# Kernel optimization log

Measured on AMD Instinct MI355X. Metric: run time of the kernel, lower is better.

The kernel has to match this reference:

```python
import jax, jax.numpy as jnp
import numpy as np
import math

BSZ, H, P, L = 8, 512, 256, 4096
DT_MIN, DT_MAX = 1e-3, 1e-1


def setup_inputs() -> dict:
    key = jax.random.key(0)
    ks = jax.random.split(key, 7)
    input_sequence = jax.random.normal(ks[0], (BSZ, 1, H, 1, L), dtype=jnp.float32)
    # HiPPO-like init: negative real parts, spread imaginary parts
    Lambda_re = -(0.1 + jax.random.uniform(ks[1], (P,), dtype=jnp.float32))  # in (-1.1, -0.1)
    Lambda_im = jax.random.normal(ks[2], (P,), dtype=jnp.float32) * math.pi
    B = jax.random.normal(ks[3], (P, H, 2), dtype=jnp.float32) / math.sqrt(H)
    C = jax.random.normal(ks[4], (H, P, 2), dtype=jnp.float32) * (0.5 ** 0.5)
    D = jax.random.normal(ks[5], (H,), dtype=jnp.float32)
    u = jax.random.uniform(ks[6], (P, 1), dtype=jnp.float32)
    log_step = math.log(DT_MIN) + u * (math.log(DT_MAX) - math.log(DT_MIN))
    return {"input_sequence": input_sequence, "Lambda_re": Lambda_re,
            "Lambda_im": Lambda_im, "B": B, "C": C, "D": D, "log_step": log_step}


def _binary_operator(q_i, q_j):
    A_i, b_i = q_i
    A_j, b_j = q_j
    return (A_j * A_i, A_j * b_i + b_j)


def reference(input_sequence, Lambda_re, Lambda_im, B, C, D, log_step):
    # conj_sym=True, clip_eigs=False, activation='gelu'
    Lambda = Lambda_re + 1j * Lambda_im                       # (P,) complex
    B_tilde = B[..., 0] + 1j * B[..., 1]                      # (P,H)
    C_tilde = C[..., 0] + 1j * C[..., 1]                      # (H,P)
    step = jnp.exp(log_step[:, 0])                            # (P,)
    # ZOH discretization
    Lambda_bar = jnp.exp(Lambda * step)                       # (P,)
    B_bar = ((Lambda_bar - 1.0) / Lambda)[:, None] * B_tilde  # (P,H)
    # (bsz,1,H,1,L) -> (bsz,L,H)
    u = input_sequence[:, 0, :, 0].transpose(0, 2, 1)
    Bu = jnp.einsum('ph,blh->blp', B_bar, u.astype(B_bar.dtype))  # (bsz,L,P) complex
    Lambda_elems = jnp.broadcast_to(Lambda_bar, Bu.shape)
    _, xs = jax.lax.associative_scan(_binary_operator, (Lambda_elems, Bu), axis=1)
    ys = 2.0 * jnp.einsum('hp,blp->blh', C_tilde, xs).real    # conj_sym output
    ys = ys + u * D                                           # feedthrough
    ys = jax.nn.gelu(ys, approximate=False)
    return ys.transpose(0, 2, 1)[:, None, :, None, :]         # (bsz,1,H,1,L)
```

## Files before the change

### kernel.cpp

```cpp
#include <hip/hip_runtime.h>
#include <math.h>

#define HH 512
#define PP 256
#define LL 4096
#define NB 8
#define BM 128
#define BN 128
#define BK 32
#define KTILES (HH / BK)

typedef __attribute__((ext_vector_type(4))) float f32x4;
typedef __attribute__((ext_vector_type(8))) __bf16 bf16x8;
typedef __attribute__((ext_vector_type(4))) unsigned short us4;
typedef __attribute__((ext_vector_type(8))) unsigned short us8;


__device__ __forceinline__ unsigned short f2bf(float x) {
  unsigned int u = __builtin_bit_cast(unsigned int, x);
  return (unsigned short)((u + 0x7fffu + ((u >> 16) & 1u)) >> 16);
}
__device__ __forceinline__ float bf2f(unsigned short h) {
  unsigned int u = ((unsigned int)h) << 16;
  return __builtin_bit_cast(float, u);
}
__device__ __forceinline__ float gelu_exact(float x) {
  return 0.5f * x * (1.0f + erff(x * 0.70710678118654752f));
}
__device__ __forceinline__ void gl_lds16(const void* g, void* l) {
  __builtin_amdgcn_global_load_lds(
      (const __attribute__((address_space(1))) unsigned int*)g,
      (__attribute__((address_space(3))) unsigned int*)l, 16, 0, 0);
}

__global__ __launch_bounds__(256) void precompute_params(
    const float* __restrict__ Lre, const float* __restrict__ Lim,
    const float* __restrict__ Bmat, const float* __restrict__ Cmat,
    const float* __restrict__ logstep,
    unsigned short* __restrict__ M1, unsigned short* __restrict__ C2,
    float* __restrict__ lam)
{
  const int p = blockIdx.x;
  const int t = threadIdx.x;
  const float re = Lre[p], im = Lim[p];
  const float step = expf(logstep[p]);
  const float er  = expf(re * step);
  const float lbr = er * cosf(im * step);
  const float lbi = er * sinf(im * step);
  if (t == 0) { lam[2*p] = lbr; lam[2*p+1] = lbi; }
  const float den = re*re + im*im;
  const float nr = lbr - 1.0f, ni = lbi;
  const float gr = (nr*re + ni*im) / den;
  const float gi = (ni*re - nr*im) / den;
  for (int h = t; h < HH; h += 256) {
    const float br = Bmat[(p*HH + h)*2 + 0];
    const float bi = Bmat[(p*HH + h)*2 + 1];
    M1[p*HH + h]        = f2bf(gr*br - gi*bi);
    M1[(PP+p)*HH + h]   = f2bf(gr*bi + gi*br);
    const float cr = Cmat[(h*PP + p)*2 + 0];
    const float ci = Cmat[(h*PP + p)*2 + 1];
    C2[h*(2*PP) + p]      = f2bf( 2.0f * cr);
    C2[h*(2*PP) + PP + p] = f2bf(-2.0f * ci);
  }
}

template<bool SRCF32, bool EPI>
__global__ __launch_bounds__(256, 4) void s5_gemm_fused(
    const unsigned short* __restrict__ A,
    const void* __restrict__ Bsrc,
    void* __restrict__ Cout,
    const float* __restrict__ Dv,
    const float* __restrict__ Ug)
{
  const int nbx = LL / BN;
  const int nby = HH / BM;
  const int nwg = nbx * nby * NB;
  const int hw  = blockIdx.x + nbx * (blockIdx.y + nby * blockIdx.z);
  const int bid = (hw & 7) * (nwg >> 3) + (hw >> 3);
  const int bx = bid % nbx;
  const int by = (bid / nbx) % nby;
  const int b  = bid / (nbx * nby);

  const int n0 = bx * BN;
  const int m0 = by * BM;
  const int tid  = threadIdx.x;
  const int lane = tid & 63;
  const int w    = tid >> 6;
  const int lr = lane & 15, lg = lane >> 4;
  const int wm = (w >> 1) * 64, wn = (w & 1) * 64;

  __shared__ __align__(16) unsigned short LB[4 * BM * BK];
  unsigned short* const As0 = LB;
  unsigned short* const Bs0 = LB + 2 * BM * BK;
#define ASEL(s) (As0 + (s) * BM * BK)
#define BSEL(s) (Bs0 + (s) * BN * BK)

  f32x4 acc[4][4];
#pragma unroll
  for (int i = 0; i < 4; ++i)
#pragma unroll
    for (int j = 0; j < 4; ++j) acc[i][j] = f32x4{0.0f, 0.0f, 0.0f, 0.0f};

  const int swz = (lg ^ ((lr >> 2) & 3)) * 8;

  const int nq = tid & 31;
  const int ko = tid >> 5;

  const float*          BsF = (const float*)Bsrc          + (size_t)b * HH * LL;
  const unsigned short* BsH = (const unsigned short*)Bsrc + (size_t)b * HH * LL;

  f32x4 bv[4];
  us4   bh[4];

#define STAGE_A(k0, sel)                                                       \
  {                                                                            \
    _Pragma("unroll")                                                          \
    for (int i = 0; i < 2; ++i) {                                              \
      const int c   = i * 256 + tid;                                           \
      const int row = c >> 2;                                                  \
      const int ks  = (c & 3) ^ ((c >> 4) & 3);                                \
      gl_lds16(A + (size_t)(m0 + row) * HH + (k0) + ks * 8, &ASEL(sel)[c * 8]);\
    }                                                                          \
  }

#define B_LOAD(k0)                                                             \
  {                                                                            \
    _Pragma("unroll")                                                          \
    for (int r = 0; r < 4; ++r) {                                              \
      if (SRCF32)                                                              \
        bv[r] = *(const f32x4*)(BsF + (size_t)((k0) + ko * 4 + r) * LL + n0 + nq * 4); \
      else                                                                     \
        bh[r] = *(const us4*)(BsH + (size_t)((k0) + ko * 4 + r) * LL + n0 + nq * 4);   \
    }                                                                          \
  }

#define B_WRITE(sel)                                                           \
  {                                                                            \
    _Pragma("unroll")                                                          \
    for (int j = 0; j < 4; ++j) {                                              \
      const int n2 = nq * 4 + j;                                               \
      us4 wv;                                                                  \
      _Pragma("unroll")                                                        \
      for (int r = 0; r < 4; ++r)                                              \
        wv[r] = SRCF32 ? f2bf(bv[r][j]) : bh[r][j];                            \
      const int slot = (ko >> 1) ^ ((n2 >> 2) & 3);                            \
      *(us4*)&BSEL(sel)[n2 * BK + slot * 8 + (ko & 1) * 4] = wv;               \
    }                                                                          \
  }

  B_LOAD(0);
  STAGE_A(0, 0);
  B_WRITE(0);
  __syncthreads();

  for (int t = 0; t < KTILES; ++t) {
    const int cur = t & 1;
    const bool more = (t + 1 < KTILES);
    if (more) {
      B_LOAD((t + 1) * BK);
      if (cur) STAGE_A((t + 1) * BK, 0) else STAGE_A((t + 1) * BK, 1);
      asm volatile("s_waitcnt vmcnt(6)" ::: "memory");
    } else {
      asm volatile("s_waitcnt vmcnt(0)" ::: "memory");
    }
    __builtin_amdgcn_sched_barrier(0);
    __builtin_amdgcn_s_barrier();
    __builtin_amdgcn_sched_barrier(0);

    bf16x8 aF[4], bF[4];
#pragma unroll
    for (int f = 0; f < 4; ++f) {
      aF[f] = *(const bf16x8*)&ASEL(cur)[(wm + f * 16 + lr) * BK + swz];
      bF[f] = *(const bf16x8*)&BSEL(cur)[(wn + f * 16 + lr) * BK + swz];
    }
#pragma unroll
    for (int fm = 0; fm < 4; ++fm)
#pragma unroll
      for (int fn = 0; fn < 4; ++fn)
        acc[fm][fn] = __builtin_amdgcn_mfma_f32_16x16x32_bf16(
            aF[fm], bF[fn], acc[fm][fn], 0, 0, 0);
    if (more) {
      if (cur) B_WRITE(0) else B_WRITE(1);
    }
    asm volatile("s_waitcnt lgkmcnt(0)" ::: "memory");
    __builtin_amdgcn_sched_barrier(0);
    __builtin_amdgcn_s_barrier();
    __builtin_amdgcn_sched_barrier(0);
  }
#undef STAGE_A
#undef B_LOAD
#undef B_WRITE

  if (!EPI) {
#pragma unroll
    for (int fm = 0; fm < 4; ++fm)
#pragma unroll
      for (int r = 0; r < 4; ++r) {
        const int row = wm + fm * 16 + lg * 4 + r;
#pragma unroll
        for (int fn = 0; fn < 4; ++fn) {
          const int col = wn + fn * 16 + lr;
          LB[row * 128 + col] = f2bf(acc[fm][fn][r]);
        }
      }
    __syncthreads();
    unsigned short* C = (unsigned short*)Cout + (size_t)b * HH * LL;
#pragma unroll
    for (int pass = 0; pass < 8; ++pass) {
      const int chunk = pass * 256 + tid;
      const int row = chunk >> 4;
      const int c8  = chunk & 15;
      us8 v = *(const us8*)&LB[row * 128 + c8 * 8];
      *(us8*)(C + (size_t)(m0 + row) * LL + n0 + c8 * 8) = v;
    }
  } else {
    float* C = (float*)Cout + (size_t)b * HH * LL;
    const float* Ub = Ug + (size_t)b * HH * LL;
#pragma unroll
    for (int fm = 0; fm < 4; ++fm)
#pragma unroll
      for (int r = 0; r < 4; ++r) {
        const int row = m0 + wm + fm*16 + lg*4 + r;
        const float dv = Dv[row];
#pragma unroll
        for (int fn = 0; fn < 4; ++fn) {
          const int col = n0 + wn + fn*16 + lr;
          const float y = fmaf(dv, Ub[(size_t)row * LL + col], acc[fm][fn][r]);
          C[(size_t)row * LL + col] = gelu_exact(y);
        }
      }
  }
#undef ASEL
#undef BSEL
}

__global__ __launch_bounds__(256) void s5_scan(
    unsigned short* __restrict__ Bu, const float* __restrict__ lam)
{
  const int p = blockIdx.x;
  const int b = blockIdx.y;
  const int t = threadIdx.x;
  const int lane = t & 63;
  const int w    = t >> 6;
  unsigned short* rowr = Bu + ((size_t)b*2*PP + p)      * LL;
  unsigned short* rowi = Bu + ((size_t)b*2*PP + PP + p) * LL;

  const float lre = lam[2*p], lim = lam[2*p+1];

  float br[16], bi[16];
  {
    us8 v0 = *(const us8*)&rowr[t*16];
    us8 v1 = *(const us8*)&rowr[t*16 + 8];
    us8 w0 = *(const us8*)&rowi[t*16];
    us8 w1 = *(const us8*)&rowi[t*16 + 8];
#pragma unroll
    for (int j = 0; j < 8; ++j) {
      br[j] = bf2f(v0[j]); br[8+j] = bf2f(v1[j]);
      bi[j] = bf2f(w0[j]); bi[8+j] = bf2f(w1[j]);
    }
  }

  float xr = 0.0f, xi = 0.0f;
#pragma unroll
  for (int j = 0; j < 16; ++j) {
    const float nr = fmaf(lre, xr, fmaf(-lim, xi, br[j]));
    const float ni = fmaf(lre, xi, fmaf( lim, xr, bi[j]));
    xr = nr; xi = ni;
  }

  float mre = lre, mim = lim;
#pragma unroll
  for (int s = 0; s < 4; ++s) {
    const float n2 = mre*mre - mim*mim;
    mim = 2.0f*mre*mim; mre = n2;
  }

  float Sr = xr, Si = xi;
  float pwr[6], pwi[6];
#pragma unroll
  for (int rnd = 0; rnd < 6; ++rnd) {
    pwr[rnd] = mre; pwi[rnd] = mim;
    const int off = 1 << rnd;
    const float vr = __shfl_up(Sr, off);
    const float vi = __shfl_up(Si, off);
    if (lane >= off) {
      Sr = fmaf(mre, vr, fmaf(-mim, vi, Sr));
      Si = fmaf(mre, vi, fmaf( mim, vr, Si));
    }
    const float n2 = mre*mre - mim*mim;
    mim = 2.0f*mre*mim; mre = n2;
  }

  __shared__ float Twr[4], Twi[4];
  if (lane == 63) { Twr[w] = Sr; Twi[w] = Si; }
  __syncthreads();

  float cwr = 0.0f, cwi = 0.0f;
  for (int v = 0; v < w; ++v) {
    const float nr = fmaf(mre, cwr, fmaf(-mim, cwi, Twr[v]));
    const float ni = fmaf(mre, cwi, fmaf( mim, cwr, Twi[v]));
    cwr = nr; cwi = ni;
  }

  float Er = __shfl_up(Sr, 1);
  float Ei = __shfl_up(Si, 1);
  if (lane == 0) { Er = 0.0f; Ei = 0.0f; }

  float plr = 1.0f, pli = 0.0f;
#pragma unroll
  for (int rnd = 0; rnd < 6; ++rnd) {
    if ((lane >> rnd) & 1) {
      const float nr = plr*pwr[rnd] - pli*pwi[rnd];
      const float ni = plr*pwi[rnd] + pli*pwr[rnd];
      plr = nr; pli = ni;
    }
  }

  const float cr = Er + plr*cwr - pli*cwi;
  const float ci = Ei + plr*cwi + pli*cwr;

  xr = cr; xi = ci;
  us8 o0, o1, o2, o3;
#pragma unroll
  for (int j = 0; j < 16; ++j) {
    const float nr = fmaf(lre, xr, fmaf(-lim, xi, br[j]));
    const float ni = fmaf(lre, xi, fmaf( lim, xr, bi[j]));
    xr = nr; xi = ni;
    if (j < 8) { o0[j] = f2bf(xr); o2[j] = f2bf(xi); }
    else       { o1[j-8] = f2bf(xr); o3[j-8] = f2bf(xi); }
  }
  *(us8*)&rowr[t*16]     = o0;
  *(us8*)&rowr[t*16 + 8] = o1;
  *(us8*)&rowi[t*16]     = o2;
  *(us8*)&rowi[t*16 + 8] = o3;
}

extern "C" void kernel_launch(void* const* d_in, const int* in_sizes, int n_in,
                              void* d_out, int out_size, void* d_ws, size_t ws_size,
                              hipStream_t stream) {
  (void)in_sizes; (void)n_in; (void)out_size; (void)ws_size;
  const float* in_seq = (const float*)d_in[0];
  const float* Lre    = (const float*)d_in[1];
  const float* Lim    = (const float*)d_in[2];
  const float* Bm     = (const float*)d_in[3];
  const float* Cm     = (const float*)d_in[4];
  const float* Dv     = (const float*)d_in[5];
  const float* ls     = (const float*)d_in[6];
  float* out = (float*)d_out;

  char* ws = (char*)d_ws;
  unsigned short* M1  = (unsigned short*)(ws);
  unsigned short* C2  = (unsigned short*)(ws + (512u << 10));
  float*          lam = (float*)(ws + (1u << 20));
  unsigned short* Bu  = (unsigned short*)(ws + (2u << 20));

  precompute_params<<<dim3(PP), dim3(256), 0, stream>>>(Lre, Lim, Bm, Cm, ls, M1, C2, lam);

  dim3 gg(LL/BN, HH/BM, NB);
  s5_gemm_fused<true, false><<<gg, dim3(256), 0, stream>>>(M1, in_seq, Bu, nullptr, nullptr);

  s5_scan<<<dim3(PP, NB), dim3(256), 0, stream>>>(Bu, lam);

  s5_gemm_fused<false, true><<<gg, dim3(256), 0, stream>>>(C2, Bu, out, Dv, in_seq);
}
```

Measured before the change: 103.7 us.

## Double GEMM K-tile and load A fragments directly from global into registers

Raises the K tile from 32 to 64, which halves the number of loop iterations and barriers. The A operand (the small weight matrix) no longer goes through LDS via global_load_lds; each wave reads its fragments straight from global memory into registers. The B tile's LDS layout gets a new 8-way XOR swizzle with 16-byte writes, and the explicit vmcnt wait is gone. In exchange, register pressure goes up (8 B vectors and 8 A fragments), and the A loads now sit just before the barrier, which may stall on global latency.

New measurement: 140.1 us. 1.35x slower.

```diff
diff --git a/kernel.cpp b/kernel.cpp
--- a/kernel.cpp
+++ b/kernel.cpp
@@ -7,7 +7,7 @@
 #define NB 8
 #define BM 128
 #define BN 128
-#define BK 32
+#define BK 64
 #define KTILES (HH / BK)
 
 typedef __attribute__((ext_vector_type(4))) float f32x4;
@@ -26,11 +26,6 @@
 }
 __device__ __forceinline__ float gelu_exact(float x) {
   return 0.5f * x * (1.0f + erff(x * 0.70710678118654752f));
-}
-__device__ __forceinline__ void gl_lds16(const void* g, void* l) {
-  __builtin_amdgcn_global_load_lds(
-      (const __attribute__((address_space(1))) unsigned int*)g,
-      (__attribute__((address_space(3))) unsigned int*)l, 16, 0, 0);
 }
 
 __global__ __launch_bounds__(256) void precompute_params(
@@ -89,19 +84,14 @@
   const int lr = lane & 15, lg = lane >> 4;
   const int wm = (w >> 1) * 64, wn = (w & 1) * 64;
 
-  __shared__ __align__(16) unsigned short LB[4 * BM * BK];
-  unsigned short* const As0 = LB;
-  unsigned short* const Bs0 = LB + 2 * BM * BK;
-#define ASEL(s) (As0 + (s) * BM * BK)
-#define BSEL(s) (Bs0 + (s) * BN * BK)
+  __shared__ __align__(16) unsigned short LB[2 * BN * BK];
+#define BSEL(s) (LB + (s) * BN * BK)
 
   f32x4 acc[4][4];
 #pragma unroll
   for (int i = 0; i < 4; ++i)
 #pragma unroll
     for (int j = 0; j < 4; ++j) acc[i][j] = f32x4{0.0f, 0.0f, 0.0f, 0.0f};
-
-  const int swz = (lg ^ ((lr >> 2) & 3)) * 8;
 
   const int nq = tid & 31;
   const int ko = tid >> 5;
@@ -109,28 +99,30 @@
   const float*          BsF = (const float*)Bsrc          + (size_t)b * HH * LL;
   const unsigned short* BsH = (const unsigned short*)Bsrc + (size_t)b * HH * LL;
 
-  f32x4 bv[4];
-  us4   bh[4];
-
-#define STAGE_A(k0, sel)                                                       \
+  f32x4 bv[8];
+  us4   bh[8];
+
+  const unsigned short* Arow = A + (size_t)(m0 + wm + lr) * HH;
+  bf16x8 aF[4][2];
+
+#define A_LOAD(k0)                                                             \
   {                                                                            \
     _Pragma("unroll")                                                          \
-    for (int i = 0; i < 2; ++i) {                                              \
-      const int c   = i * 256 + tid;                                           \
-      const int row = c >> 2;                                                  \
-      const int ks  = (c & 3) ^ ((c >> 4) & 3);                                \
-      gl_lds16(A + (size_t)(m0 + row) * HH + (k0) + ks * 8, &ASEL(sel)[c * 8]);\
-    }                                                                          \
+    for (int f = 0; f < 4; ++f)                                                \
+      _Pragma("unroll")                                                        \
+      for (int kk = 0; kk < 2; ++kk)                                           \
+        aF[f][kk] = *(const bf16x8*)(Arow + (size_t)(f * 16) * HH + (k0) +     \
+                                     (kk * 4 + lg) * 8);                       \
   }
 
 #define B_LOAD(k0)                                                             \
   {                                                                            \
     _Pragma("unroll")                                                          \
-    for (int r = 0; r < 4; ++r) {                                              \
+    for (int r = 0; r < 8; ++r) {                                              \
       if (SRCF32)                                                              \
-        bv[r] = *(const f32x4*)(BsF + (size_t)((k0) + ko * 4 + r) * LL + n0 + nq * 4); \
+        bv[r] = *(const f32x4*)(BsF + (size_t)((k0) + ko * 8 + r) * LL + n0 + nq * 4); \
       else                                                                     \
-        bh[r] = *(const us4*)(BsH + (size_t)((k0) + ko * 4 + r) * LL + n0 + nq * 4);   \
+        bh[r] = *(const us4*)(BsH + (size_t)((k0) + ko * 8 + r) * LL + n0 + nq * 4);   \
     }                                                                          \
   }
 
@@ -139,47 +131,40 @@
     _Pragma("unroll")                                                          \
     for (int j = 0; j < 4; ++j) {                                              \
       const int n2 = nq * 4 + j;                                               \
-      us4 wv;                                                                  \
+      us8 wv;                                                                  \
       _Pragma("unroll")                                                        \
-      for (int r = 0; r < 4; ++r)                                              \
+      for (int r = 0; r < 8; ++r)                                              \
         wv[r] = SRCF32 ? f2bf(bv[r][j]) : bh[r][j];                            \
-      const int slot = (ko >> 1) ^ ((n2 >> 2) & 3);                            \
-      *(us4*)&BSEL(sel)[n2 * BK + slot * 8 + (ko & 1) * 4] = wv;               \
+      *(us8*)&BSEL(sel)[n2 * BK + ((ko ^ (n2 & 7)) * 8)] = wv;                 \
     }                                                                          \
   }
 
   B_LOAD(0);
-  STAGE_A(0, 0);
+  A_LOAD(0);
   B_WRITE(0);
   __syncthreads();
 
   for (int t = 0; t < KTILES; ++t) {
     const int cur = t & 1;
     const bool more = (t + 1 < KTILES);
+    if (more) B_LOAD((t + 1) * BK);
+
+#pragma unroll
+    for (int fn = 0; fn < 4; ++fn) {
+      const int rb = (wn + fn * 16 + lr) * BK;
+      bf16x8 bF0 = *(const bf16x8*)&BSEL(cur)[rb + ((0 * 4 + lg) ^ (lr & 7)) * 8];
+      bf16x8 bF1 = *(const bf16x8*)&BSEL(cur)[rb + ((1 * 4 + lg) ^ (lr & 7)) * 8];
+#pragma unroll
+      for (int fm = 0; fm < 4; ++fm) {
+        acc[fm][fn] = __builtin_amdgcn_mfma_f32_16x16x32_bf16(
+            aF[fm][0], bF0, acc[fm][fn], 0, 0, 0);
+        acc[fm][fn] = __builtin_amdgcn_mfma_f32_16x16x32_bf16(
+            aF[fm][1], bF1, acc[fm][fn], 0, 0, 0);
+      }
+    }
+
     if (more) {
-      B_LOAD((t + 1) * BK);
-      if (cur) STAGE_A((t + 1) * BK, 0) else STAGE_A((t + 1) * BK, 1);
-      asm volatile("s_waitcnt vmcnt(6)" ::: "memory");
-    } else {
-      asm volatile("s_waitcnt vmcnt(0)" ::: "memory");
-    }
-    __builtin_amdgcn_sched_barrier(0);
-    __builtin_amdgcn_s_barrier();
-    __builtin_amdgcn_sched_barrier(0);
-
-    bf16x8 aF[4], bF[4];
-#pragma unroll
-    for (int f = 0; f < 4; ++f) {
-      aF[f] = *(const bf16x8*)&ASEL(cur)[(wm + f * 16 + lr) * BK + swz];
-      bF[f] = *(const bf16x8*)&BSEL(cur)[(wn + f * 16 + lr) * BK + swz];
-    }
-#pragma unroll
-    for (int fm = 0; fm < 4; ++fm)
-#pragma unroll
-      for (int fn = 0; fn < 4; ++fn)
-        acc[fm][fn] = __builtin_amdgcn_mfma_f32_16x16x32_bf16(
-            aF[fm], bF[fn], acc[fm][fn], 0, 0, 0);
-    if (more) {
+      A_LOAD((t + 1) * BK);
       if (cur) B_WRITE(0) else B_WRITE(1);
     }
     asm volatile("s_waitcnt lgkmcnt(0)" ::: "memory");
@@ -187,7 +172,7 @@
     __builtin_amdgcn_s_barrier();
     __builtin_amdgcn_sched_barrier(0);
   }
-#undef STAGE_A
+#undef A_LOAD
 #undef B_LOAD
 #undef B_WRITE
 
@@ -230,7 +215,6 @@
         }
       }
   }
-#undef ASEL
 #undef BSEL
 }
 
```

## Prefetch B tiles two steps ahead with double register buffers in GEMM loop

Applied to the files above, without the earlier changes.

The main GEMM K-loop now keeps two sets of B-operand registers, so the global load for tile t+2 is issued while tile t+1's registers are still waiting to be written to LDS. The loop is unrolled by two with a hand-written two-tile epilogue. Fragment loads are also reordered: all four B fragments are loaded up front and the A fragment is loaded per row-block. The aim is to hide more global-load latency behind the MFMA work. In exchange it uses more VGPRs, which may lower occupancy, and the vmcnt wait counts must stay correct for the loads in flight.

Measured after the change: 183.3 us. +76.8%, slower.

```diff
diff --git a/kernel.cpp b/kernel.cpp
--- a/kernel.cpp
+++ b/kernel.cpp
@@ -109,8 +109,8 @@
   const float*          BsF = (const float*)Bsrc          + (size_t)b * HH * LL;
   const unsigned short* BsH = (const unsigned short*)Bsrc + (size_t)b * HH * LL;
 
-  f32x4 bv[4];
-  us4   bh[4];
+  f32x4 bvA[4], bvB[4];
+  us4   bhA[4], bhB[4];
 
 #define STAGE_A(k0, sel)                                                       \
   {                                                                            \
@@ -123,18 +123,18 @@
     }                                                                          \
   }
 
-#define B_LOAD(k0)                                                             \
+#define B_LOAD(k0, RF, RH)                                                     \
   {                                                                            \
     _Pragma("unroll")                                                          \
     for (int r = 0; r < 4; ++r) {                                              \
       if (SRCF32)                                                              \
-        bv[r] = *(const f32x4*)(BsF + (size_t)((k0) + ko * 4 + r) * LL + n0 + nq * 4); \
+        RF[r] = *(const f32x4*)(BsF + (size_t)((k0) + ko * 4 + r) * LL + n0 + nq * 4); \
       else                                                                     \
-        bh[r] = *(const us4*)(BsH + (size_t)((k0) + ko * 4 + r) * LL + n0 + nq * 4);   \
+        RH[r] = *(const us4*)(BsH + (size_t)((k0) + ko * 4 + r) * LL + n0 + nq * 4);   \
     }                                                                          \
   }
 
-#define B_WRITE(sel)                                                           \
+#define B_WRITE(sel, RF, RH)                                                   \
   {                                                                            \
     _Pragma("unroll")                                                          \
     for (int j = 0; j < 4; ++j) {                                              \
@@ -142,54 +142,73 @@
       us4 wv;                                                                  \
       _Pragma("unroll")                                                        \
       for (int r = 0; r < 4; ++r)                                              \
-        wv[r] = SRCF32 ? f2bf(bv[r][j]) : bh[r][j];                            \
+        wv[r] = SRCF32 ? f2bf(RF[r][j]) : RH[r][j];                            \
       const int slot = (ko >> 1) ^ ((n2 >> 2) & 3);                            \
       *(us4*)&BSEL(sel)[n2 * BK + slot * 8 + (ko & 1) * 4] = wv;               \
     }                                                                          \
   }
 
-  B_LOAD(0);
+#define COMPUTE(CUR)                                                           \
+  {                                                                            \
+    bf16x8 bF[4];                                                              \
+    _Pragma("unroll")                                                          \
+    for (int f = 0; f < 4; ++f)                                                \
+      bF[f] = *(const bf16x8*)&BSEL(CUR)[(wn + f * 16 + lr) * BK + swz];       \
+    _Pragma("unroll")                                                          \
+    for (int fm = 0; fm < 4; ++fm) {                                           \
+      bf16x8 aF = *(const bf16x8*)&ASEL(CUR)[(wm + fm * 16 + lr) * BK + swz];  \
+      _Pragma("unroll")                                                        \
+      for (int fn = 0; fn < 4; ++fn)                                           \
+        acc[fm][fn] = __builtin_amdgcn_mfma_f32_16x16x32_bf16(                 \
+            aF, bF[fn], acc[fm][fn], 0, 0, 0);                                 \
+    }                                                                          \
+  }
+
+#define SB __builtin_amdgcn_sched_barrier(0)
+#define BAR __builtin_amdgcn_s_barrier()
+
+  B_LOAD(0, bvA, bhA);
   STAGE_A(0, 0);
-  B_WRITE(0);
+  B_WRITE(0, bvA, bhA);
+  B_LOAD(BK, bvA, bhA);
   __syncthreads();
 
-  for (int t = 0; t < KTILES; ++t) {
-    const int cur = t & 1;
-    const bool more = (t + 1 < KTILES);
-    if (more) {
-      B_LOAD((t + 1) * BK);
-      if (cur) STAGE_A((t + 1) * BK, 0) else STAGE_A((t + 1) * BK, 1);
-      asm volatile("s_waitcnt vmcnt(6)" ::: "memory");
-    } else {
-      asm volatile("s_waitcnt vmcnt(0)" ::: "memory");
-    }
-    __builtin_amdgcn_sched_barrier(0);
-    __builtin_amdgcn_s_barrier();
-    __builtin_amdgcn_sched_barrier(0);
-
-    bf16x8 aF[4], bF[4];
-#pragma unroll
-    for (int f = 0; f < 4; ++f) {
-      aF[f] = *(const bf16x8*)&ASEL(cur)[(wm + f * 16 + lr) * BK + swz];
-      bF[f] = *(const bf16x8*)&BSEL(cur)[(wn + f * 16 + lr) * BK + swz];
-    }
-#pragma unroll
-    for (int fm = 0; fm < 4; ++fm)
-#pragma unroll
-      for (int fn = 0; fn < 4; ++fn)
-        acc[fm][fn] = __builtin_amdgcn_mfma_f32_16x16x32_bf16(
-            aF[fm], bF[fn], acc[fm][fn], 0, 0, 0);
-    if (more) {
-      if (cur) B_WRITE(0) else B_WRITE(1);
-    }
-    asm volatile("s_waitcnt lgkmcnt(0)" ::: "memory");
-    __builtin_amdgcn_sched_barrier(0);
-    __builtin_amdgcn_s_barrier();
-    __builtin_amdgcn_sched_barrier(0);
-  }
+#define STEP_FULL(T, CUR, RFu, RHu, RFf, RHf)                                  \
+  {                                                                            \
+    B_LOAD(((T) + 2) * BK, RFf, RHf);                                          \
+    STAGE_A(((T) + 1) * BK, (CUR) ^ 1);                                        \
+    asm volatile("s_waitcnt vmcnt(6)" ::: "memory");                           \
+    SB; BAR; SB;                                                               \
+    COMPUTE(CUR);                                                              \
+    B_WRITE((CUR) ^ 1, RFu, RHu);                                              \
+    asm volatile("s_waitcnt lgkmcnt(0)" ::: "memory");                         \
+    SB; BAR; SB;                                                               \
+  }
+
+  for (int t = 0; t < KTILES - 2; t += 2) {
+    STEP_FULL(t,     0, bvA, bhA, bvB, bhB);
+    STEP_FULL(t + 1, 1, bvB, bhB, bvA, bhA);
+  }
+
+  STAGE_A((KTILES - 1) * BK, 1);
+  asm volatile("s_waitcnt vmcnt(2)" ::: "memory");
+  SB; BAR; SB;
+  COMPUTE(0);
+  B_WRITE(1, bvA, bhA);
+  asm volatile("s_waitcnt lgkmcnt(0)" ::: "memory");
+  SB; BAR; SB;
+  asm volatile("s_waitcnt vmcnt(0)" ::: "memory");
+  SB; BAR; SB;
+  COMPUTE(1);
+  SB; BAR;
+
+#undef STEP_FULL
 #undef STAGE_A
 #undef B_LOAD
 #undef B_WRITE
+#undef COMPUTE
+#undef SB
+#undef BAR
 
   if (!EPI) {
 #pragma unroll
```

## Single-buffer B tile in LDS, raise occupancy hint, drop LDS-staged epilogue

Applied to the files above, without the earlier changes.

The B operand tile moves from double-buffered to single-buffered LDS, which cuts shared memory per block by a quarter. The launch-bounds occupancy hint rises from 4 to 6 waves-per-EU blocks. An extra barrier now separates the MFMA reads from the next B write. The bf16 output epilogue writes directly from registers to global memory instead of staging through LDS for coalesced 16-byte stores. The goal is more resident workgroups to hide latency, at the cost of an extra barrier per k-tile, uncoalesced 2-byte stores, and possible register pressure or spills under the tighter bound.

Result: slower. 344.9 us (+232.7%).

```diff
diff --git a/kernel.cpp b/kernel.cpp
--- a/kernel.cpp
+++ b/kernel.cpp
@@ -65,7 +65,7 @@
 }
 
 template<bool SRCF32, bool EPI>
-__global__ __launch_bounds__(256, 4) void s5_gemm_fused(
+__global__ __launch_bounds__(256, 6) void s5_gemm_fused(
     const unsigned short* __restrict__ A,
     const void* __restrict__ Bsrc,
     void* __restrict__ Cout,
@@ -89,11 +89,9 @@
   const int lr = lane & 15, lg = lane >> 4;
   const int wm = (w >> 1) * 64, wn = (w & 1) * 64;
 
-  __shared__ __align__(16) unsigned short LB[4 * BM * BK];
-  unsigned short* const As0 = LB;
-  unsigned short* const Bs0 = LB + 2 * BM * BK;
-#define ASEL(s) (As0 + (s) * BM * BK)
-#define BSEL(s) (Bs0 + (s) * BN * BK)
+  __shared__ __align__(16) unsigned short LB[3 * BM * BK];
+  unsigned short* const Bs = LB + 2 * BM * BK;
+#define ASEL(s) (LB + (s) * BM * BK)
 
   f32x4 acc[4][4];
 #pragma unroll
@@ -134,7 +132,7 @@
     }                                                                          \
   }
 
-#define B_WRITE(sel)                                                           \
+#define B_WRITE()                                                              \
   {                                                                            \
     _Pragma("unroll")                                                          \
     for (int j = 0; j < 4; ++j) {                                              \
@@ -144,13 +142,16 @@
       for (int r = 0; r < 4; ++r)                                              \
         wv[r] = SRCF32 ? f2bf(bv[r][j]) : bh[r][j];                            \
       const int slot = (ko >> 1) ^ ((n2 >> 2) & 3);                            \
-      *(us4*)&BSEL(sel)[n2 * BK + slot * 8 + (ko & 1) * 4] = wv;               \
+      *(us4*)&Bs[n2 * BK + slot * 8 + (ko & 1) * 4] = wv;                      \
     }                                                                          \
   }
+
+#define SB __builtin_amdgcn_sched_barrier(0)
+#define BAR __builtin_amdgcn_s_barrier()
 
   B_LOAD(0);
   STAGE_A(0, 0);
-  B_WRITE(0);
+  B_WRITE();
   __syncthreads();
 
   for (int t = 0; t < KTILES; ++t) {
@@ -163,15 +164,13 @@
     } else {
       asm volatile("s_waitcnt vmcnt(0)" ::: "memory");
     }
-    __builtin_amdgcn_sched_barrier(0);
-    __builtin_amdgcn_s_barrier();
-    __builtin_amdgcn_sched_barrier(0);
+    SB; BAR; SB;
 
     bf16x8 aF[4], bF[4];
 #pragma unroll
     for (int f = 0; f < 4; ++f) {
       aF[f] = *(const bf16x8*)&ASEL(cur)[(wm + f * 16 + lr) * BK + swz];
-      bF[f] = *(const bf16x8*)&BSEL(cur)[(wn + f * 16 + lr) * BK + swz];
+      bF[f] = *(const bf16x8*)&Bs[(wn + f * 16 + lr) * BK + swz];
     }
 #pragma unroll
     for (int fm = 0; fm < 4; ++fm)
@@ -179,40 +178,33 @@
       for (int fn = 0; fn < 4; ++fn)
         acc[fm][fn] = __builtin_amdgcn_mfma_f32_16x16x32_bf16(
             aF[fm], bF[fn], acc[fm][fn], 0, 0, 0);
+
+    SB; BAR; SB;
     if (more) {
-      if (cur) B_WRITE(0) else B_WRITE(1);
-    }
-    asm volatile("s_waitcnt lgkmcnt(0)" ::: "memory");
-    __builtin_amdgcn_sched_barrier(0);
-    __builtin_amdgcn_s_barrier();
-    __builtin_amdgcn_sched_barrier(0);
+      B_WRITE();
+      asm volatile("s_waitcnt lgkmcnt(0)" ::: "memory");
+      SB;
+    }
   }
 #undef STAGE_A
 #undef B_LOAD
 #undef B_WRITE
+#undef SB
+#undef BAR
 
   if (!EPI) {
+    unsigned short* C = (unsigned short*)Cout + (size_t)b * HH * LL;
 #pragma unroll
     for (int fm = 0; fm < 4; ++fm)
 #pragma unroll
       for (int r = 0; r < 4; ++r) {
-        const int row = wm + fm * 16 + lg * 4 + r;
+        const int row = m0 + wm + fm*16 + lg*4 + r;
 #pragma unroll
         for (int fn = 0; fn < 4; ++fn) {
-          const int col = wn + fn * 16 + lr;
-          LB[row * 128 + col] = f2bf(acc[fm][fn][r]);
+          const int col = n0 + wn + fn*16 + lr;
+          C[(size_t)row * LL + col] = f2bf(acc[fm][fn][r]);
         }
       }
-    __syncthreads();
-    unsigned short* C = (unsigned short*)Cout + (size_t)b * HH * LL;
-#pragma unroll
-    for (int pass = 0; pass < 8; ++pass) {
-      const int chunk = pass * 256 + tid;
-      const int row = chunk >> 4;
-      const int c8  = chunk & 15;
-      us8 v = *(const us8*)&LB[row * 128 + c8 * 8];
-      *(us8*)(C + (size_t)(m0 + row) * LL + n0 + c8 * 8) = v;
-    }
   } else {
     float* C = (float*)Cout + (size_t)b * HH * LL;
     const float* Ub = Ug + (size_t)b * HH * LL;
@@ -231,7 +223,6 @@
       }
   }
 #undef ASEL
-#undef BSEL
 }
 
 __global__ __launch_bounds__(256) void s5_scan(
```
